# Kernel optimization log

Measured on AMD Instinct MI355X. Metric: run time of the kernel, lower is better.

The kernel has to match this reference:

```python
import jax, jax.numpy as jnp
import numpy as np

RADIX = 23                 # hidden_radix fixed-point fractional bits
SCALE = float(1 << RADIX)
F = 10                     # fractional bits used to quantize forget gates
FS = 1 << F
MAX_FORGET = 0.875
H = 512
D = H // 2
SLICE = 100
VOCAB = 32000
T, B = 512, 64
L = 2


def setup_inputs() -> dict:
    key = jax.random.key(0)
    ks = jax.random.split(key, 8)
    s = 0.06  # ~1/sqrt(768) init scale, keeps gates unsaturated
    return {
        "input_seq": jax.random.randint(ks[0], (T, B), 0, VOCAB),
        "lengths": jax.random.randint(ks[1], (B,), 1, T + 1),
        "emb": jax.random.normal(ks[2], (VOCAB, H), jnp.float32) * s,
        "Wz1": jax.random.normal(ks[3], (L, H + D, H), jnp.float32) * s,
        "bz1": jnp.zeros((L, H), jnp.float32),
        "Wg1": jax.random.normal(ks[4], (L, H + D, D), jnp.float32) * s,
        "bg1": jnp.zeros((L, D), jnp.float32),
        "Wz2": jax.random.normal(ks[5], (L, H + D, H), jnp.float32) * s,
        "bz2": jnp.zeros((L, H), jnp.float32),
        "Wg2": jax.random.normal(ks[6], (L, H + D, D), jnp.float32) * s,
        "bg2": jnp.zeros((L, D), jnp.float32),
    }


def _to_float(h_int):
    # ConvertToFloat: dequantize int fixed-point hidden (radix 23)
    return h_int.astype(jnp.float32) / SCALE


def _quant_gate(z):
    # restrict forgetting: z in [1 - max_forget, 1], then quantize to F frac bits
    z = MAX_FORGET * z + (1.0 - MAX_FORGET)
    return jnp.clip(jnp.floor(z * FS), 1, FS).astype(jnp.int32)


def _fixed_mul(h, zq):
    # exact floor(h * zq / 2**F) in int32 (no overflow): split h into hi/lo
    h_hi = h >> F               # arithmetic shift == floor division
    h_lo = h & (FS - 1)
    return h_hi * zq + ((h_lo * zq) >> F)


def _revgru_cell(x, h, Wz1, bz1, Wg1, bg1, Wz2, bz2, Wg2, bg2):
    # h: int32 [B, H] fixed-point hidden, split into reversible halves
    h1, h2 = h[:, :D], h[:, D:]
    h2f = _to_float(h2)
    zr1 = jax.nn.sigmoid(jnp.concatenate([x, h2f], 1) @ Wz1 + bz1)   # [B, H]
    zq1, r1 = _quant_gate(zr1[:, :D]), zr1[:, D:]
    z1f = zq1.astype(jnp.float32) / FS
    g1 = jnp.tanh(jnp.concatenate([x, r1 * h2f], 1) @ Wg1 + bg1)     # [B, D]
    h1 = _fixed_mul(h1, zq1) + jnp.round((1.0 - z1f) * g1 * SCALE).astype(jnp.int32)
    h1f = _to_float(h1)
    zr2 = jax.nn.sigmoid(jnp.concatenate([x, h1f], 1) @ Wz2 + bz2)
    zq2, r2 = _quant_gate(zr2[:, :D]), zr2[:, D:]
    z2f = zq2.astype(jnp.float32) / FS
    g2 = jnp.tanh(jnp.concatenate([x, r2 * h1f], 1) @ Wg2 + bg2)
    h2 = _fixed_mul(h2, zq2) + jnp.round((1.0 - z2f) * g2 * SCALE).astype(jnp.int32)
    return jnp.concatenate([h1, h2], 1)


def reference(input_seq, lengths, emb, Wz1, bz1, Wg1, bg1, Wz2, bz2, Wg2, bg2):
    input_seq = input_seq.astype(jnp.int32)
    xs = emb[input_seq]                                       # [T, B, H] (lockdropi p=0)
    mask = jnp.arange(T)[:, None] < lengths[None, :]          # [T, B]
    h0 = jnp.zeros((B, H), jnp.int32)
    cur = xs
    last_hiddens = []
    all_hs = None
    # stacked RNN: run each layer fully over time (equivalent to the t,l double loop)
    for l in range(L):
        def step(h, inp, l=l):
            x, m = inp
            hn = _revgru_cell(x, h, Wz1[l], bz1[l], Wg1[l], bg1[l],
                              Wz2[l], bz2[l], Wg2[l], bg2[l])
            hn = jnp.where(m[:, None], hn, h)                 # length masking
            return hn, hn
        hT, hs = jax.lax.scan(step, h0, (cur, mask))
        last_hiddens.append(hT)
        if l < L - 1:
            cur = _to_float(hs)                               # output_hidden (lockdroph p=0)
        else:
            all_hs = hs
    # saved_hiddens: top-layer hidden slice before each step plus final -> T+1 entries
    saved = jnp.concatenate([h0[None], all_hs], 0)[:, :, :SLICE]
    return jnp.stack(last_hiddens), saved
```

## Files before the change

kernel.cpp:

```cpp
#include <hip/hip_runtime.h>
#include <stdint.h>


typedef __attribute__((ext_vector_type(8))) short short8;
typedef __attribute__((ext_vector_type(4))) float floatx4;

#define MFMA16(a,b,c) __builtin_amdgcn_mfma_f32_16x16x32_bf16((a),(b),(c),0,0,0)

__device__ __forceinline__ short bf16_rne(float f) {
  uint32_t u = __float_as_uint(f);
  u += 0x7FFFu + ((u >> 16) & 1u);
  return (short)(u >> 16);
}
__device__ __forceinline__ float bf16f(short s) {
  return __uint_as_float(((uint32_t)(uint16_t)s) << 16);
}
__device__ __forceinline__ void st64(unsigned long long* p, unsigned long long v) {
  __hip_atomic_store(p, v, __ATOMIC_RELAXED, __HIP_MEMORY_SCOPE_AGENT);
}
__device__ __forceinline__ unsigned long long ld64(const unsigned long long* p) {
  return __hip_atomic_load(p, __ATOMIC_RELAXED, __HIP_MEMORY_SCOPE_AGENT);
}

#define SCALE_F 8388608.0f
#define INV_S   (1.0f/8388608.0f)

__device__ float g_X[50331648];
__device__ short g_WTh[2][786432];
__device__ short g_WTl[2][786432];
__device__ float g_biasL[2][1536];
__device__ unsigned long long g_ch[2][4][6][4096];
__device__ unsigned long long g_h0s[16777216];
__device__ unsigned long long g_x1r[3145728];
__device__ unsigned long long g_sent[2][4][4][8];
__device__ unsigned g_epoch;

__global__ void bump_epoch() { g_epoch = g_epoch + 1u; }

__global__ void prep_x(const float* __restrict__ Wz1, const float* __restrict__ bz1,
                       const float* __restrict__ Wg1, const float* __restrict__ bg1,
                       const float* __restrict__ Wz2, const float* __restrict__ bz2,
                       const float* __restrict__ Wg2, const float* __restrict__ bg2,
                       int layer, int* __restrict__ d_out, int zero_extra) {
  int idx = blockIdx.x * 256 + threadIdx.x;
  int k = idx / 1536;
  int c = idx - k * 1536;
  const float* W; const float* bb; int cc; int ncols;
  if (c < 512)       { W = Wz1; bb = bz1; cc = c;        ncols = 512; }
  else if (c < 768)  { W = Wg1; bb = bg1; cc = c - 512;  ncols = 256; }
  else if (c < 1280) { W = Wz2; bb = bz2; cc = c - 768;  ncols = 512; }
  else               { W = Wg2; bb = bg2; cc = c - 1280; ncols = 256; }
  float wv = W[(size_t)layer * 768 * ncols + (size_t)k * ncols + cc];
  short hi = bf16_rne(wv);
  short lo = bf16_rne(wv - bf16f(hi));
  g_WTh[layer][(size_t)c * 512 + k] = hi;
  g_WTl[layer][(size_t)c * 512 + k] = lo;
  if (k == 0) g_biasL[layer][c] = bb[layer * ncols + cc];
  if (zero_extra && idx < 6400) d_out[65536 + idx] = 0;
}

__global__ __launch_bounds__(256)
void gemmx_kernel(const int* __restrict__ seq, const float* __restrict__ emb) {
  __shared__ float At[128][36];
  __shared__ short Bhi[128][40];
  __shared__ short Blo[128][40];
  __shared__ int toks[128];
  int tid = threadIdx.x;
  int r0 = blockIdx.x * 128;
  int c0 = blockIdx.y * 128;
  if (tid < 128) toks[tid] = seq[r0 + tid];
  int lane = tid & 63;
  int wid = tid >> 6;
  int wm = wid & 1, wn = wid >> 1;
  int lm = lane & 15, lq = lane >> 4;
  floatx4 zero4 = {0.f, 0.f, 0.f, 0.f};
  floatx4 acc[4][4];
#pragma unroll
  for (int a = 0; a < 4; ++a)
#pragma unroll
    for (int b = 0; b < 4; ++b) acc[a][b] = zero4;
  __syncthreads();
  int am = tid >> 1;
  int ah = (tid & 1) * 16;
  const float* arow = emb + (size_t)toks[am] * 512;
  const short* bh_base = g_WTh[0] + (size_t)(c0 + am) * 512;
  const short* bl_base = g_WTl[0] + (size_t)(c0 + am) * 512;
  for (int kb = 0; kb < 16; ++kb) {
    int k0 = kb * 32 + ah;
    float4 a0 = *(const float4*)(arow + k0);
    float4 a1 = *(const float4*)(arow + k0 + 4);
    float4 a2 = *(const float4*)(arow + k0 + 8);
    float4 a3 = *(const float4*)(arow + k0 + 12);
    short4 b0 = *(const short4*)(bh_base + k0);
    short4 b1 = *(const short4*)(bh_base + k0 + 4);
    short4 b2 = *(const short4*)(bh_base + k0 + 8);
    short4 b3 = *(const short4*)(bh_base + k0 + 12);
    short4 l0 = *(const short4*)(bl_base + k0);
    short4 l1 = *(const short4*)(bl_base + k0 + 4);
    short4 l2 = *(const short4*)(bl_base + k0 + 8);
    short4 l3 = *(const short4*)(bl_base + k0 + 12);
    __syncthreads();
    *(float4*)&At[am][ah]      = a0;
    *(float4*)&At[am][ah + 4]  = a1;
    *(float4*)&At[am][ah + 8]  = a2;
    *(float4*)&At[am][ah + 12] = a3;
    *(short4*)&Bhi[am][ah]      = b0;
    *(short4*)&Bhi[am][ah + 4]  = b1;
    *(short4*)&Bhi[am][ah + 8]  = b2;
    *(short4*)&Bhi[am][ah + 12] = b3;
    *(short4*)&Blo[am][ah]      = l0;
    *(short4*)&Blo[am][ah + 4]  = l1;
    *(short4*)&Blo[am][ah + 8]  = l2;
    *(short4*)&Blo[am][ah + 12] = l3;
    __syncthreads();
    short8 afh[4], afl[4];
#pragma unroll
    for (int mt = 0; mt < 4; ++mt) {
      const float* ap = &At[wm*64 + mt*16 + lm][lq*8];
#pragma unroll
      for (int j = 0; j < 8; ++j) {
        float v = ap[j];
        short hi = bf16_rne(v);
        afh[mt][j] = hi;
        afl[mt][j] = bf16_rne(v - bf16f(hi));
      }
    }
#pragma unroll
    for (int nt = 0; nt < 4; ++nt) {
      short8 bfh = *(short8*)&Bhi[wn*64 + nt*16 + lm][lq*8];
      short8 bfl = *(short8*)&Blo[wn*64 + nt*16 + lm][lq*8];
#pragma unroll
      for (int mt = 0; mt < 4; ++mt) {
        acc[mt][nt] = MFMA16(afh[mt], bfh, acc[mt][nt]);
        acc[mt][nt] = MFMA16(afl[mt], bfh, acc[mt][nt]);
        acc[mt][nt] = MFMA16(afh[mt], bfl, acc[mt][nt]);
      }
    }
  }
#pragma unroll
  for (int nt = 0; nt < 4; ++nt) {
    int gc = c0 + wn*64 + nt*16 + lm;
    float bv = g_biasL[0][gc];
#pragma unroll
    for (int mt = 0; mt < 4; ++mt) {
#pragma unroll
      for (int i = 0; i < 4; ++i) {
        int gr = r0 + wm*64 + mt*16 + lq*4 + i;
        g_X[(size_t)gr * 1536 + gc] = acc[mt][nt][i] + bv;
      }
    }
  }
}

__global__ __launch_bounds__(512, 2)
void fused_kernel(const float* __restrict__ Wz1g, const float* __restrict__ Wg1g,
                  const float* __restrict__ Wz2g, const float* __restrict__ Wg2g,
                  const int* __restrict__ lengths, int* __restrict__ d_out) {
  __shared__ int   h1i[16][260];
  __shared__ int   h2i[16][260];
  __shared__ short phi[16][264];
  __shared__ short pmi[16][264];
  __shared__ short plo[16][264];
  __shared__ float redbuf[2304];
  __shared__ int lens[16];
  __shared__ short ahs[16][520];
  __shared__ short als[16][520];

  int tid = threadIdx.x;
  int bid = blockIdx.x;
  int lane = tid & 63, wv = tid >> 6;
  int lm = lane & 15, lq = lane >> 4;
  unsigned ep = g_epoch;

  if (bid >= 64) {
    int xw = bid - 64;
    int r4 = xw & 3;
    int cs = xw >> 2;
    int colx = cs * 128 + wv * 16 + lm;
    short8 bh[16], bl[16];
#pragma unroll
    for (int kf = 0; kf < 16; ++kf) {
      bh[kf] = *(const short8*)&g_WTh[1][(size_t)colx * 512 + kf * 32 + lq * 8];
      bl[kf] = *(const short8*)&g_WTl[1][(size_t)colx * 512 + kf * 32 + lq * 8];
    }
    float bvx = g_biasL[1][colx];
    int sr2 = tid >> 5;
    int cb  = (tid & 31) * 16;

    for (int t = 0; t < 512; ++t) {
      unsigned tagt = (ep << 10) | (unsigned)(t + 1);
      if (tid < 8) {
        const unsigned long long* sp = &g_sent[0][r4][3][tid];
        while ((int)((unsigned)(ld64(sp) >> 32) - tagt) < 0) __builtin_amdgcn_s_sleep(2);
      }
      __syncthreads();
      {
        const unsigned long long* hp = &g_h0s[((size_t)(t * 64) + r4 * 16 + sr2) * 512 + cb];
        unsigned long long v[16];
        do { v[0] = ld64(hp); } while ((unsigned)(v[0] >> 32) != tagt);
#pragma unroll
        for (int i = 1; i < 16; ++i) v[i] = ld64(hp + i);
        unsigned pend = 0;
#pragma unroll
        for (int i = 1; i < 16; ++i)
          if ((unsigned)(v[i] >> 32) != tagt) pend |= 1u << i;
        while (pend) {
          __builtin_amdgcn_s_sleep(1);
#pragma unroll
          for (int i = 1; i < 16; ++i)
            if (pend & (1u << i)) {
              v[i] = ld64(hp + i);
              if ((unsigned)(v[i] >> 32) == tagt) pend &= ~(1u << i);
            }
        }
#pragma unroll
        for (int i = 0; i < 16; ++i) {
          float f = __uint_as_float((unsigned)v[i]);
          short hi = bf16_rne(f);
          ahs[sr2][cb + i] = hi;
          als[sr2][cb + i] = bf16_rne(f - bf16f(hi));
        }
      }
      __syncthreads();
      floatx4 acc = {0.f, 0.f, 0.f, 0.f};
#pragma unroll
      for (int kf = 0; kf < 16; ++kf) {
        short8 a0 = *(short8*)&ahs[lm][kf * 32 + lq * 8];
        short8 a1 = *(short8*)&als[lm][kf * 32 + lq * 8];
        acc = MFMA16(a0, bh[kf], acc);
        acc = MFMA16(a1, bh[kf], acc);
        acc = MFMA16(a0, bl[kf], acc);
      }
      if (t >= 25) {
        if (tid < 4) {
          unsigned need = (ep << 10) | (unsigned)(t - 24);
          while ((unsigned)(ld64(&g_ch[1][tid][5][0]) >> 32) < need) __builtin_amdgcn_s_sleep(2);
        }
      }
      __syncthreads();
#pragma unroll
      for (int i = 0; i < 4; ++i) {
        int row = r4 * 16 + lq * 4 + i;
        st64(&g_x1r[((size_t)(t & 31) * 64 + row) * 1536 + colx],
             ((unsigned long long)tagt << 32) | __float_as_uint(acc[i] + bvx));
      }
      __syncthreads();
    }
    return;
  }

  int grp = bid & 7;
  int cg  = bid >> 3;
  int L   = grp >> 2;
  int dm  = grp & 3;
  int rb0 = dm * 16;
  unsigned long long (*ch)[4096] = g_ch[L][dm];

  if (tid < 16) lens[tid] = lengths[rb0 + tid];
  for (int i = tid; i < 16 * 260; i += 512) { ((int*)h1i)[i] = 0; ((int*)h2i)[i] = 0; }

  short8 wz1a[4], wz1b[4], wz1c[4], wz2a[4], wz2b[4], wz2c[4];
  short8 wg1a[2], wg1b[2], wg2a[2], wg2b[2];
  {
    int nt = wv & 3, kh = wv >> 2;
    int colz = cg * 64 + nt * 16 + lm;
    const float* W1 = Wz1g + (size_t)L * 768 * 512 + (size_t)512 * 512 + colz;
    const float* W2 = Wz2g + (size_t)L * 768 * 512 + (size_t)512 * 512 + colz;
#pragma unroll
    for (int ks = 0; ks < 4; ++ks) {
      int k0 = kh * 128 + ks * 32 + lq * 8;
      short8 t0, t1, t2, u0, u1, u2;
#pragma unroll
      for (int j = 0; j < 8; ++j) {
        float v = W1[(size_t)(k0 + j) * 512] * INV_S;
        short a0 = bf16_rne(v); float r1 = v - bf16f(a0);
        short a1 = bf16_rne(r1); float r2 = r1 - bf16f(a1);
        t0[j] = a0; t1[j] = a1; t2[j] = bf16_rne(r2);
        float v2 = W2[(size_t)(k0 + j) * 512] * INV_S;
        short d0 = bf16_rne(v2); float s1 = v2 - bf16f(d0);
        short d1 = bf16_rne(s1); float s2 = s1 - bf16f(d1);
        u0[j] = d0; u1[j] = d1; u2[j] = bf16_rne(s2);
      }
      wz1a[ks] = t0; wz1b[ks] = t1; wz1c[ks] = t2;
      wz2a[ks] = u0; wz2b[ks] = u1; wz2c[ks] = u2;
    }
    int ntg = wv & 1, kq = wv >> 1;
    int colg = cg * 32 + ntg * 16 + lm;
    const float* G1 = Wg1g + (size_t)L * 768 * 256 + (size_t)512 * 256 + colg;
    const float* G2 = Wg2g + (size_t)L * 768 * 256 + (size_t)512 * 256 + colg;
#pragma unroll
    for (int ks = 0; ks < 2; ++ks) {
      int k0 = kq * 64 + ks * 32 + lq * 8;
      short8 t0, t1, u0, u1;
#pragma unroll
      for (int j = 0; j < 8; ++j) {
        float v = G1[(size_t)(k0 + j) * 256];
        short a0 = bf16_rne(v);
        t0[j] = a0; t1[j] = bf16_rne(v - bf16f(a0));
        float v2 = G2[(size_t)(k0 + j) * 256];
        short d0 = bf16_rne(v2);
        u0[j] = d0; u1[j] = bf16_rne(v2 - bf16f(d0));
      }
      wg1a[ks] = t0; wg1b[ks] = t1; wg2a[ks] = u0; wg2b[ks] = u1;
    }
  }
  __syncthreads();

  int xr = tid & 15, xc = tid >> 4;
  int sr = tid >> 5, sc0 = (tid & 31) << 3;

  auto ldx = [&](int tt, float& za, float& zb, float& g1x, float& ya, float& yb, float& g2x) {
    const float* base = g_X + (size_t)(tt * 64 + rb0 + xr) * 1536;
    float2 v1 = *(const float2*)(base + cg * 64 + 2 * xc);
    za = v1.x; zb = v1.y;
    g1x = base[512 + cg * 32 + xc];
    float2 v2 = *(const float2*)(base + 768 + cg * 64 + 2 * xc);
    ya = v2.x; yb = v2.y;
    g2x = base[1280 + cg * 32 + xc];
  };
  float cz1a = 0.f, cz1b = 0.f, cg1x = 0.f, cz2a = 0.f, cz2b = 0.f, cg2x = 0.f;
  if (L == 0) ldx(0, cz1a, cz1b, cg1x, cz2a, cz2b, cg2x);

#define GATE(PH, NEED)                                                         \
  {                                                                            \
    if (tid < 8) {                                                             \
      const unsigned long long* sp_ = &g_sent[L][dm][PH][tid];                 \
      while ((int)((unsigned)(ld64(sp_) >> 32) - (NEED)) < 0)                  \
        __builtin_amdgcn_s_sleep(2);                                           \
    }                                                                          \
    __syncthreads();                                                           \
  }

#define STAGE8(CHIDX, EXP, DEPOSIT)                                            \
  {                                                                            \
    const unsigned long long* cp_ = &ch[CHIDX][sr * 256 + sc0];                \
    unsigned long long v_[8];                                                  \
    do { v_[0] = ld64(cp_); } while ((unsigned)(v_[0] >> 32) != (EXP));        \
    _Pragma("unroll")                                                          \
    for (int i_ = 1; i_ < 8; ++i_) v_[i_] = ld64(cp_ + i_);                    \
    unsigned pend_ = 0;                                                        \
    _Pragma("unroll")                                                          \
    for (int i_ = 1; i_ < 8; ++i_)                                             \
      if ((unsigned)(v_[i_] >> 32) != (EXP)) pend_ |= 1u << i_;                \
    while (pend_) {                                                            \
      __builtin_amdgcn_s_sleep(1);                                             \
      _Pragma("unroll")                                                        \
      for (int i_ = 1; i_ < 8; ++i_)                                           \
        if (pend_ & (1u << i_)) {                                              \
          v_[i_] = ld64(cp_ + i_);                                             \
          if ((unsigned)(v_[i_] >> 32) == (EXP)) pend_ &= ~(1u << i_);         \
        }                                                                      \
    }                                                                          \
    _Pragma("unroll")                                                          \
    for (int i_ = 0; i_ < 8; ++i_) { DEPOSIT; }                                \
  }

#define SPLIT3(SRC)                                                            \
  {                                                                            \
    _Pragma("unroll")                                                          \
    for (int i_ = 0; i_ < 8; ++i_) {                                           \
      float v = (float)SRC[sr][sc0 + i_];                                      \
      short a0 = bf16_rne(v); float r1 = v - bf16f(a0);                        \
      short a1 = bf16_rne(r1); float r2 = r1 - bf16f(a1);                      \
      phi[sr][sc0 + i_] = a0; pmi[sr][sc0 + i_] = a1;                          \
      plo[sr][sc0 + i_] = bf16_rne(r2);                                       \
    }                                                                          \
  }

  for (int t = 0; t < 512; ++t) {
    unsigned tagp = (ep << 10) | (unsigned)(t + 1);
    auto rdx = [&](int col) -> float {
      const unsigned long long* p = &g_x1r[((size_t)(t & 31) * 64 + rb0 + xr) * 1536 + col];
      unsigned long long v;
      do { v = ld64(p); } while ((unsigned)(v >> 32) != tagp);
      return __uint_as_float((unsigned)v);
    };
    float nz1a, nz1b, ng1x, nz2a, nz2b, ng2x;
    if (L == 0) {
      int tn = (t + 1 < 512) ? t + 1 : t;
      ldx(tn, nz1a, nz1b, ng1x, nz2a, nz2b, ng2x);
    }

    if (t > 0) {
      GATE(3, (ep << 10) | (unsigned)t);
      STAGE8(5, (ep << 10) | (unsigned)t, h2i[sr][sc0 + i_] = (int)(unsigned)v_[i_]);
    }
    SPLIT3(h2i);
    __syncthreads();
    {
      int nt = wv & 3, kh = wv >> 2;
      floatx4 acc = {0.f, 0.f, 0.f, 0.f};
#pragma unroll
      for (int ks = 0; ks < 4; ++ks) {
        int k0 = kh * 128 + ks * 32 + lq * 8;
        short8 a0 = *(short8*)&phi[lm][k0];
        short8 a1 = *(short8*)&pmi[lm][k0];
        short8 a2 = *(short8*)&plo[lm][k0];
        acc = MFMA16(a0, wz1a[ks], acc);
        acc = MFMA16(a0, wz1b[ks], acc);
        acc = MFMA16(a1, wz1a[ks], acc);
        acc = MFMA16(a1, wz1b[ks], acc);
        acc = MFMA16(a0, wz1c[ks], acc);
        acc = MFMA16(a2, wz1a[ks], acc);
      }
#pragma unroll
      for (int i = 0; i < 4; ++i) redbuf[kh * 1088 + (lq * 4 + i) * 68 + nt * 16 + lm] = acc[i];
    }
    __syncthreads();
    {
      if (L == 1) { cz1a = rdx(cg * 64 + 2 * xc); cz1b = rdx(cg * 64 + 2 * xc + 1); }
#pragma unroll
      for (int u = 0; u < 2; ++u) {
        int cc = 2 * xc + u;
        float pre = redbuf[xr * 68 + cc] + redbuf[1088 + xr * 68 + cc] + (u ? cz1b : cz1a);
        float s = 1.0f / (1.0f + expf(-pre));
        int gcol = cg * 64 + cc;
        if (gcol < 256) {
          float qf = floorf((0.875f * s + 0.125f) * 1024.0f);
          int qi = (int)qf; qi = qi < 1 ? 1 : (qi > 1024 ? 1024 : qi);
          st64(&ch[0][xr * 256 + gcol], ((unsigned long long)tagp << 32) | (unsigned)qi);
        } else {
          int rc = gcol - 256;
          float p = s * ((float)h2i[xr][rc] * INV_S);
          short p0 = bf16_rne(p);
          short p1s = bf16_rne(p - bf16f(p0));
          unsigned pay = ((unsigned)(unsigned short)p0 << 16) | (unsigned)(unsigned short)p1s;
          st64(&ch[1][xr * 256 + rc], ((unsigned long long)tagp << 32) | pay);
        }
      }
    }
    __syncthreads();
    if (tid == 0) st64(&g_sent[L][dm][0][cg], ((unsigned long long)tagp << 32) | 1u);
    GATE(0, tagp);

    int qv;
    STAGE8(1, tagp, { unsigned pl_ = (unsigned)v_[i_];
                      phi[sr][sc0 + i_] = (short)(pl_ >> 16);
                      plo[sr][sc0 + i_] = (short)(pl_ & 0xFFFFu); });
    {
      const unsigned long long* qp = &ch[0][xr * 256 + cg * 32 + xc];
      unsigned long long q64;
      do { q64 = ld64(qp); } while ((unsigned)(q64 >> 32) != tagp);
      qv = (int)(unsigned)q64;
    }
    __syncthreads();
    {
      int ntg = wv & 1, kq = wv >> 1;
      floatx4 acc = {0.f, 0.f, 0.f, 0.f};
#pragma unroll
      for (int ks = 0; ks < 2; ++ks) {
        int k0 = kq * 64 + ks * 32 + lq * 8;
        short8 a0 = *(short8*)&phi[lm][k0];
        short8 a1 = *(short8*)&plo[lm][k0];
        acc = MFMA16(a0, wg1a[ks], acc);
        acc = MFMA16(a1, wg1a[ks], acc);
        acc = MFMA16(a0, wg1b[ks], acc);
      }
#pragma unroll
      for (int i = 0; i < 4; ++i) redbuf[kq * 576 + (lq * 4 + i) * 36 + ntg * 16 + lm] = acc[i];
    }
    __syncthreads();
    {
      if (L == 1) cg1x = rdx(512 + cg * 32 + xc);
      float pre = redbuf[xr * 36 + xc] + redbuf[576 + xr * 36 + xc]
                + redbuf[1152 + xr * 36 + xc] + redbuf[1728 + xr * 36 + xc] + cg1x;
      float g = tanhf(pre);
      int gc = cg * 32 + xc;
      int q = qv;
      int hold = h1i[xr][gc];
      float zf = (float)q * (1.0f / 1024.0f);
      int ni = (int)rintf((1.0f - zf) * g * SCALE_F);
      int hnew = (hold >> 10) * q + (((hold & 1023) * q) >> 10) + ni;
      if (t >= lens[xr]) hnew = hold;
      st64(&ch[2][xr * 256 + gc], ((unsigned long long)tagp << 32) | (unsigned)hnew);
      if (L == 0)
        st64(&g_h0s[((size_t)(t * 64) + rb0 + xr) * 512 + gc],
             ((unsigned long long)tagp << 32) | __float_as_uint((float)hnew * INV_S));
      else if (gc < 100) d_out[65536 + (t + 1) * 6400 + (rb0 + xr) * 100 + gc] = hnew;
      if (t == 511) d_out[L * 32768 + (rb0 + xr) * 512 + gc] = hnew;
    }
    __syncthreads();
    if (tid == 0) st64(&g_sent[L][dm][1][cg], ((unsigned long long)tagp << 32) | 1u);
    GATE(1, tagp);

    STAGE8(2, tagp, h1i[sr][sc0 + i_] = (int)(unsigned)v_[i_]);
    SPLIT3(h1i);
    __syncthreads();
    {
      int nt = wv & 3, kh = wv >> 2;
      floatx4 acc = {0.f, 0.f, 0.f, 0.f};
#pragma unroll
      for (int ks = 0; ks < 4; ++ks) {
        int k0 = kh * 128 + ks * 32 + lq * 8;
        short8 a0 = *(short8*)&phi[lm][k0];
        short8 a1 = *(short8*)&pmi[lm][k0];
        short8 a2 = *(short8*)&plo[lm][k0];
        acc = MFMA16(a0, wz2a[ks], acc);
        acc = MFMA16(a0, wz2b[ks], acc);
        acc = MFMA16(a1, wz2a[ks], acc);
        acc = MFMA16(a1, wz2b[ks], acc);
        acc = MFMA16(a0, wz2c[ks], acc);
        acc = MFMA16(a2, wz2a[ks], acc);
      }
#pragma unroll
      for (int i = 0; i < 4; ++i) redbuf[kh * 1088 + (lq * 4 + i) * 68 + nt * 16 + lm] = acc[i];
    }
    __syncthreads();
    {
      if (L == 1) { cz2a = rdx(768 + cg * 64 + 2 * xc); cz2b = rdx(768 + cg * 64 + 2 * xc + 1); }
#pragma unroll
      for (int u = 0; u < 2; ++u) {
        int cc = 2 * xc + u;
        float pre = redbuf[xr * 68 + cc] + redbuf[1088 + xr * 68 + cc] + (u ? cz2b : cz2a);
        float s = 1.0f / (1.0f + expf(-pre));
        int gcol = cg * 64 + cc;
        if (gcol < 256) {
          float qf = floorf((0.875f * s + 0.125f) * 1024.0f);
          int qi = (int)qf; qi = qi < 1 ? 1 : (qi > 1024 ? 1024 : qi);
          st64(&ch[3][xr * 256 + gcol], ((unsigned long long)tagp << 32) | (unsigned)qi);
        } else {
          int rc = gcol - 256;
          float p = s * ((float)h1i[xr][rc] * INV_S);
          short p0 = bf16_rne(p);
          short p1s = bf16_rne(p - bf16f(p0));
          unsigned pay = ((unsigned)(unsigned short)p0 << 16) | (unsigned)(unsigned short)p1s;
          st64(&ch[4][xr * 256 + rc], ((unsigned long long)tagp << 32) | pay);
        }
      }
    }
    __syncthreads();
    if (tid == 0) st64(&g_sent[L][dm][2][cg], ((unsigned long long)tagp << 32) | 1u);
    GATE(2, tagp);

    int qv2;
    STAGE8(4, tagp, { unsigned pl_ = (unsigned)v_[i_];
                      phi[sr][sc0 + i_] = (short)(pl_ >> 16);
                      plo[sr][sc0 + i_] = (short)(pl_ & 0xFFFFu); });
    {
      const unsigned long long* qp = &ch[3][xr * 256 + cg * 32 + xc];
      unsigned long long q64;
      do { q64 = ld64(qp); } while ((unsigned)(q64 >> 32) != tagp);
      qv2 = (int)(unsigned)q64;
    }
    __syncthreads();
    {
      int ntg = wv & 1, kq = wv >> 1;
      floatx4 acc = {0.f, 0.f, 0.f, 0.f};
#pragma unroll
      for (int ks = 0; ks < 2; ++ks) {
        int k0 = kq * 64 + ks * 32 + lq * 8;
        short8 a0 = *(short8*)&phi[lm][k0];
        short8 a1 = *(short8*)&plo[lm][k0];
        acc = MFMA16(a0, wg2a[ks], acc);
        acc = MFMA16(a1, wg2a[ks], acc);
        acc = MFMA16(a0, wg2b[ks], acc);
      }
#pragma unroll
      for (int i = 0; i < 4; ++i) redbuf[kq * 576 + (lq * 4 + i) * 36 + ntg * 16 + lm] = acc[i];
    }
    __syncthreads();
    {
      if (L == 1) cg2x = rdx(1280 + cg * 32 + xc);
      float pre = redbuf[xr * 36 + xc] + redbuf[576 + xr * 36 + xc]
                + redbuf[1152 + xr * 36 + xc] + redbuf[1728 + xr * 36 + xc] + cg2x;
      float g = tanhf(pre);
      int gc = cg * 32 + xc;
      int q = qv2;
      int hold = h2i[xr][gc];
      float zf = (float)q * (1.0f / 1024.0f);
      int ni = (int)rintf((1.0f - zf) * g * SCALE_F);
      int hnew = (hold >> 10) * q + (((hold & 1023) * q) >> 10) + ni;
      if (t >= lens[xr]) hnew = hold;
      st64(&ch[5][xr * 256 + gc], ((unsigned long long)tagp << 32) | (unsigned)hnew);
      if (L == 0)
        st64(&g_h0s[((size_t)(t * 64) + rb0 + xr) * 512 + 256 + gc],
             ((unsigned long long)tagp << 32) | __float_as_uint((float)hnew * INV_S));
      if (t == 511) d_out[L * 32768 + (rb0 + xr) * 512 + 256 + gc] = hnew;
    }
    __syncthreads();
    if (tid == 0) st64(&g_sent[L][dm][3][cg], ((unsigned long long)tagp << 32) | 1u);

    if (L == 0) {
      cz1a = nz1a; cz1b = nz1b; cg1x = ng1x; cz2a = nz2a; cz2b = nz2b; cg2x = ng2x;
    }
  }
#undef GATE
#undef STAGE8
#undef SPLIT3
}

extern "C" void kernel_launch(void* const* d_in, const int* in_sizes, int n_in,
                              void* d_out, int out_size, void* d_ws, size_t ws_size,
                              hipStream_t stream) {
  const int*   seq     = (const int*)d_in[0];
  const int*   lengths = (const int*)d_in[1];
  const float* emb     = (const float*)d_in[2];
  const float* Wz1     = (const float*)d_in[3];
  const float* bz1     = (const float*)d_in[4];
  const float* Wg1     = (const float*)d_in[5];
  const float* bg1     = (const float*)d_in[6];
  const float* Wz2     = (const float*)d_in[7];
  const float* bz2     = (const float*)d_in[8];
  const float* Wg2     = (const float*)d_in[9];
  const float* bg2     = (const float*)d_in[10];
  int* out = (int*)d_out;
  (void)in_sizes; (void)n_in; (void)out_size; (void)d_ws; (void)ws_size;

  bump_epoch<<<1, 1, 0, stream>>>();
  prep_x<<<3072, 256, 0, stream>>>(Wz1, bz1, Wg1, bg1, Wz2, bz2, Wg2, bg2, 0, out, 1);
  prep_x<<<3072, 256, 0, stream>>>(Wz1, bz1, Wg1, bg1, Wz2, bz2, Wg2, bg2, 1, out, 0);
  gemmx_kernel<<<dim3(256, 12), 256, 0, stream>>>(seq, emb);
  fused_kernel<<<112, 512, 0, stream>>>(Wz1, Wg1, Wz2, Wg2, lengths, out);
}
```

Measured before the change: 8.738 ms.

## Speculatively issue tagged channel loads before barrier polling in recurrent kernel

```diff
diff --git a/kernel.cpp b/kernel.cpp
--- a/kernel.cpp
+++ b/kernel.cpp
@@ -152,7 +152,7 @@
   }
 }
 
-__global__ __launch_bounds__(512, 2)
+__global__ __launch_bounds__(512, 1)
 void fused_kernel(const float* __restrict__ Wz1g, const float* __restrict__ Wg1g,
                   const float* __restrict__ Wz2g, const float* __restrict__ Wg2g,
                   const int* __restrict__ lengths, int* __restrict__ d_out) {
@@ -189,25 +189,24 @@
 
     for (int t = 0; t < 512; ++t) {
       unsigned tagt = (ep << 10) | (unsigned)(t + 1);
-      if (tid < 8) {
-        const unsigned long long* sp = &g_sent[0][r4][3][tid];
-        while ((int)((unsigned)(ld64(sp) >> 32) - tagt) < 0) __builtin_amdgcn_s_sleep(2);
-      }
-      __syncthreads();
       {
         const unsigned long long* hp = &g_h0s[((size_t)(t * 64) + r4 * 16 + sr2) * 512 + cb];
         unsigned long long v[16];
-        do { v[0] = ld64(hp); } while ((unsigned)(v[0] >> 32) != tagt);
-#pragma unroll
-        for (int i = 1; i < 16; ++i) v[i] = ld64(hp + i);
+#pragma unroll
+        for (int i = 0; i < 16; ++i) v[i] = ld64(hp + i);
+        if (tid < 8) {
+          const unsigned long long* sp = &g_sent[0][r4][3][tid];
+          while ((int)((unsigned)(ld64(sp) >> 32) - tagt) < 0) __builtin_amdgcn_s_sleep(2);
+        }
+        __syncthreads();
         unsigned pend = 0;
 #pragma unroll
-        for (int i = 1; i < 16; ++i)
+        for (int i = 0; i < 16; ++i)
           if ((unsigned)(v[i] >> 32) != tagt) pend |= 1u << i;
         while (pend) {
           __builtin_amdgcn_s_sleep(1);
 #pragma unroll
-          for (int i = 1; i < 16; ++i)
+          for (int i = 0; i < 16; ++i)
             if (pend & (1u << i)) {
               v[i] = ld64(hp + i);
               if ((unsigned)(v[i] >> 32) == tagt) pend &= ~(1u << i);
@@ -321,7 +320,7 @@
   float cz1a = 0.f, cz1b = 0.f, cg1x = 0.f, cz2a = 0.f, cz2b = 0.f, cg2x = 0.f;
   if (L == 0) ldx(0, cz1a, cz1b, cg1x, cz2a, cz2b, cg2x);
 
-#define GATE(PH, NEED)                                                         \
+#define GPOLL(PH, NEED)                                                        \
   {                                                                            \
     if (tid < 8) {                                                             \
       const unsigned long long* sp_ = &g_sent[L][dm][PH][tid];                 \
@@ -331,21 +330,22 @@
     __syncthreads();                                                           \
   }
 
-#define STAGE8(CHIDX, EXP, DEPOSIT)                                            \
+#define SPECLD8(CHIDX)                                                         \
+  const unsigned long long* cp_ = &ch[CHIDX][sr * 256 + sc0];                  \
+  unsigned long long v_[8];                                                    \
+  _Pragma("unroll")                                                            \
+  for (int i_ = 0; i_ < 8; ++i_) v_[i_] = ld64(cp_ + i_);
+
+#define VERIFY8(EXP, DEPOSIT)                                                  \
   {                                                                            \
-    const unsigned long long* cp_ = &ch[CHIDX][sr * 256 + sc0];                \
-    unsigned long long v_[8];                                                  \
-    do { v_[0] = ld64(cp_); } while ((unsigned)(v_[0] >> 32) != (EXP));        \
-    _Pragma("unroll")                                                          \
-    for (int i_ = 1; i_ < 8; ++i_) v_[i_] = ld64(cp_ + i_);                    \
     unsigned pend_ = 0;                                                        \
     _Pragma("unroll")                                                          \
-    for (int i_ = 1; i_ < 8; ++i_)                                             \
+    for (int i_ = 0; i_ < 8; ++i_)                                             \
       if ((unsigned)(v_[i_] >> 32) != (EXP)) pend_ |= 1u << i_;                \
     while (pend_) {                                                            \
       __builtin_amdgcn_s_sleep(1);                                             \
       _Pragma("unroll")                                                        \
-      for (int i_ = 1; i_ < 8; ++i_)                                           \
+      for (int i_ = 0; i_ < 8; ++i_)                                           \
         if (pend_ & (1u << i_)) {                                              \
           v_[i_] = ld64(cp_ + i_);                                             \
           if ((unsigned)(v_[i_] >> 32) == (EXP)) pend_ &= ~(1u << i_);         \
@@ -354,6 +354,15 @@
     _Pragma("unroll")                                                          \
     for (int i_ = 0; i_ < 8; ++i_) { DEPOSIT; }                                \
   }
+
+#define DEP_SPLIT(HARR)                                                        \
+  { int hv2_ = (int)(unsigned)v_[i_];                                          \
+    HARR[sr][sc0 + i_] = hv2_;                                                 \
+    float fv_ = (float)hv2_;                                                   \
+    short a0_ = bf16_rne(fv_); float r1_ = fv_ - bf16f(a0_);                   \
+    short a1_ = bf16_rne(r1_); float r2_ = r1_ - bf16f(a1_);                   \
+    phi[sr][sc0 + i_] = a0_; pmi[sr][sc0 + i_] = a1_;                          \
+    plo[sr][sc0 + i_] = bf16_rne(r2_); }
 
 #define SPLIT3(SRC)                                                            \
   {                                                                            \
@@ -363,29 +372,38 @@
       short a0 = bf16_rne(v); float r1 = v - bf16f(a0);                        \
       short a1 = bf16_rne(r1); float r2 = r1 - bf16f(a1);                      \
       phi[sr][sc0 + i_] = a0; pmi[sr][sc0 + i_] = a1;                          \
-      plo[sr][sc0 + i_] = bf16_rne(r2);                                       \
+      plo[sr][sc0 + i_] = bf16_rne(r2);                                        \
     }                                                                          \
   }
 
   for (int t = 0; t < 512; ++t) {
     unsigned tagp = (ep << 10) | (unsigned)(t + 1);
-    auto rdx = [&](int col) -> float {
-      const unsigned long long* p = &g_x1r[((size_t)(t & 31) * 64 + rb0 + xr) * 1536 + col];
-      unsigned long long v;
-      do { v = ld64(p); } while ((unsigned)(v >> 32) != tagp);
-      return __uint_as_float((unsigned)v);
-    };
+
     float nz1a, nz1b, ng1x, nz2a, nz2b, ng2x;
     if (L == 0) {
       int tn = (t + 1 < 512) ? t + 1 : t;
       ldx(tn, nz1a, nz1b, ng1x, nz2a, nz2b, ng2x);
     }
 
+    const unsigned long long *xq0, *xq1, *xq2, *xq3, *xq4, *xq5;
+    unsigned long long x0v = 0, x1v = 0, x2v = 0, x3v = 0, x4v = 0, x5v = 0;
+    if (L == 1) {
+      const unsigned long long* xb = &g_x1r[((size_t)((t & 31) * 64) + rb0 + xr) * 1536];
+      xq0 = xb + cg * 64 + 2 * xc;        xq1 = xq0 + 1;
+      xq2 = xb + 512 + cg * 32 + xc;
+      xq3 = xb + 768 + cg * 64 + 2 * xc;  xq4 = xq3 + 1;
+      xq5 = xb + 1280 + cg * 32 + xc;
+      x0v = ld64(xq0); x1v = ld64(xq1); x2v = ld64(xq2);
+      x3v = ld64(xq3); x4v = ld64(xq4); x5v = ld64(xq5);
+    }
+
     if (t > 0) {
-      GATE(3, (ep << 10) | (unsigned)t);
-      STAGE8(5, (ep << 10) | (unsigned)t, h2i[sr][sc0 + i_] = (int)(unsigned)v_[i_]);
-    }
-    SPLIT3(h2i);
+      SPECLD8(5)
+      GPOLL(3, (ep << 10) | (unsigned)t)
+      VERIFY8((ep << 10) | (unsigned)t, DEP_SPLIT(h2i))
+    } else {
+      SPLIT3(h2i);
+    }
     __syncthreads();
     {
       int nt = wv & 3, kh = wv >> 2;
@@ -407,8 +425,31 @@
       for (int i = 0; i < 4; ++i) redbuf[kh * 1088 + (lq * 4 + i) * 68 + nt * 16 + lm] = acc[i];
     }
     __syncthreads();
-    {
-      if (L == 1) { cz1a = rdx(cg * 64 + 2 * xc); cz1b = rdx(cg * 64 + 2 * xc + 1); }
+    if (L == 1) {
+      unsigned xp = 0;
+      if ((unsigned)(x0v >> 32) != tagp) xp |= 1u;
+      if ((unsigned)(x1v >> 32) != tagp) xp |= 2u;
+      if ((unsigned)(x2v >> 32) != tagp) xp |= 4u;
+      if ((unsigned)(x3v >> 32) != tagp) xp |= 8u;
+      if ((unsigned)(x4v >> 32) != tagp) xp |= 16u;
+      if ((unsigned)(x5v >> 32) != tagp) xp |= 32u;
+      while (xp) {
+        __builtin_amdgcn_s_sleep(1);
+        if (xp & 1u)  { x0v = ld64(xq0); if ((unsigned)(x0v >> 32) == tagp) xp &= ~1u; }
+        if (xp & 2u)  { x1v = ld64(xq1); if ((unsigned)(x1v >> 32) == tagp) xp &= ~2u; }
+        if (xp & 4u)  { x2v = ld64(xq2); if ((unsigned)(x2v >> 32) == tagp) xp &= ~4u; }
+        if (xp & 8u)  { x3v = ld64(xq3); if ((unsigned)(x3v >> 32) == tagp) xp &= ~8u; }
+        if (xp & 16u) { x4v = ld64(xq4); if ((unsigned)(x4v >> 32) == tagp) xp &= ~16u; }
+        if (xp & 32u) { x5v = ld64(xq5); if ((unsigned)(x5v >> 32) == tagp) xp &= ~32u; }
+      }
+      cz1a = __uint_as_float((unsigned)x0v);
+      cz1b = __uint_as_float((unsigned)x1v);
+      cg1x = __uint_as_float((unsigned)x2v);
+      cz2a = __uint_as_float((unsigned)x3v);
+      cz2b = __uint_as_float((unsigned)x4v);
+      cg2x = __uint_as_float((unsigned)x5v);
+    }
+    {
 #pragma unroll
       for (int u = 0; u < 2; ++u) {
         int cc = 2 * xc + u;
@@ -431,17 +472,21 @@
     }
     __syncthreads();
     if (tid == 0) st64(&g_sent[L][dm][0][cg], ((unsigned long long)tagp << 32) | 1u);
-    GATE(0, tagp);
 
     int qv;
-    STAGE8(1, tagp, { unsigned pl_ = (unsigned)v_[i_];
+    {
+      SPECLD8(1)
+      const unsigned long long* qp_ = &ch[0][xr * 256 + cg * 32 + xc];
+      unsigned long long q64_ = ld64(qp_);
+      GPOLL(0, tagp)
+      VERIFY8(tagp, { unsigned pl_ = (unsigned)v_[i_];
                       phi[sr][sc0 + i_] = (short)(pl_ >> 16);
-                      plo[sr][sc0 + i_] = (short)(pl_ & 0xFFFFu); });
-    {
-      const unsigned long long* qp = &ch[0][xr * 256 + cg * 32 + xc];
-      unsigned long long q64;
-      do { q64 = ld64(qp); } while ((unsigned)(q64 >> 32) != tagp);
-      qv = (int)(unsigned)q64;
+                      plo[sr][sc0 + i_] = (short)(pl_ & 0xFFFFu); })
+      while ((unsigned)(q64_ >> 32) != tagp) {
+        __builtin_amdgcn_s_sleep(1);
+        q64_ = ld64(qp_);
+      }
+      qv = (int)(unsigned)q64_;
     }
     __syncthreads();
     {
@@ -461,7 +506,6 @@
     }
     __syncthreads();
     {
-      if (L == 1) cg1x = rdx(512 + cg * 32 + xc);
       float pre = redbuf[xr * 36 + xc] + redbuf[576 + xr * 36 + xc]
                 + redbuf[1152 + xr * 36 + xc] + redbuf[1728 + xr * 36 + xc] + cg1x;
       float g = tanhf(pre);
@@ -481,10 +525,12 @@
     }
     __syncthreads();
     if (tid == 0) st64(&g_sent[L][dm][1][cg], ((unsigned long long)tagp << 32) | 1u);
-    GATE(1, tagp);
-
-    STAGE8(2, tagp, h1i[sr][sc0 + i_] = (int)(unsigned)v_[i_]);
-    SPLIT3(h1i);
+
+    {
+      SPECLD8(2)
+      GPOLL(1, tagp)
+      VERIFY8(tagp, DEP_SPLIT(h1i))
+    }
     __syncthreads();
     {
       int nt = wv & 3, kh = wv >> 2;
@@ -507,7 +553,6 @@
     }
     __syncthreads();
     {
-      if (L == 1) { cz2a = rdx(768 + cg * 64 + 2 * xc); cz2b = rdx(768 + cg * 64 + 2 * xc + 1); }
 #pragma unroll
       for (int u = 0; u < 2; ++u) {
         int cc = 2 * xc + u;
@@ -530,17 +575,21 @@
     }
     __syncthreads();
     if (tid == 0) st64(&g_sent[L][dm][2][cg], ((unsigned long long)tagp << 32) | 1u);
-    GATE(2, tagp);
 
     int qv2;
-    STAGE8(4, tagp, { unsigned pl_ = (unsigned)v_[i_];
+    {
+      SPECLD8(4)
+      const unsigned long long* qp_ = &ch[3][xr * 256 + cg * 32 + xc];
+      unsigned long long q64_ = ld64(qp_);
+      GPOLL(2, tagp)
+      VERIFY8(tagp, { unsigned pl_ = (unsigned)v_[i_];
                       phi[sr][sc0 + i_] = (short)(pl_ >> 16);
-                      plo[sr][sc0 + i_] = (short)(pl_ & 0xFFFFu); });
-    {
-      const unsigned long long* qp = &ch[3][xr * 256 + cg * 32 + xc];
-      unsigned long long q64;
-      do { q64 = ld64(qp); } while ((unsigned)(q64 >> 32) != tagp);
-      qv2 = (int)(unsigned)q64;
+                      plo[sr][sc0 + i_] = (short)(pl_ & 0xFFFFu); })
+      while ((unsigned)(q64_ >> 32) != tagp) {
+        __builtin_amdgcn_s_sleep(1);
+        q64_ = ld64(qp_);
+      }
+      qv2 = (int)(unsigned)q64_;
     }
     __syncthreads();
     {
@@ -560,7 +609,6 @@
     }
     __syncthreads();
     {
-      if (L == 1) cg2x = rdx(1280 + cg * 32 + xc);
       float pre = redbuf[xr * 36 + xc] + redbuf[576 + xr * 36 + xc]
                 + redbuf[1152 + xr * 36 + xc] + redbuf[1728 + xr * 36 + xc] + cg2x;
       float g = tanhf(pre);
@@ -584,8 +632,10 @@
       cz1a = nz1a; cz1b = nz1b; cg1x = ng1x; cz2a = nz2a; cz2b = nz2b; cg2x = ng2x;
     }
   }
-#undef GATE
-#undef STAGE8
+#undef GPOLL
+#undef SPECLD8
+#undef VERIFY8
+#undef DEP_SPLIT
 #undef SPLIT3
 }
 
```

Measured after the change: 12.01 ms. 1.37x slower.
